# Performance work log

Hardware: AMD Instinct MI355X
Metric: run time of the kernel (lower is better)

Reference implementation:

```python
import jax, jax.numpy as jnp
import numpy as np

B, N, M = 8, 4096, 4096

def _sqdist(x, y):
    # x: [B,N,3], y: [B,M,3] -> squared euclidean distances [B,N,M]
    return jnp.sum((x[:, :, None, :] - y[:, None, :, :]) ** 2, axis=-1)

def _approx_match(xyz1, xyz2):
    # Faithful port of Fan et al. approxmatch.cu (used by PyTorchEMD's
    # earth_mover_distance): annealed soft-assignment over 10 levels.
    b, n, _ = xyz1.shape
    m = xyz2.shape[1]
    d2 = _sqdist(xyz1, xyz2)                      # [B,N,M]
    factorl = max(n, m) / n
    factorr = max(n, m) / m
    satl = jnp.full((b, n), factorl, d2.dtype)    # remaining mass, left
    satr = jnp.full((b, m), factorr, d2.dtype)    # remaining mass, right
    match = jnp.zeros_like(d2)
    # levels: -4^7 .. -4^-1, then 0 (exactly as in approxmatch.cu)
    levels = [-(4.0 ** j) for j in range(7, -2, -1)] + [0.0]
    for level in levels:
        w = jnp.exp(level * d2) * satr[:, None, :]                 # [B,N,M]
        w = w * (satl / (jnp.sum(w, axis=2) + 1e-9))[:, :, None]   # row normalize
        ss2 = jnp.sum(w, axis=1)                                   # [B,M]
        ratio = jnp.minimum(satr / (ss2 + 1e-9), 1.0)
        w = w * ratio[:, None, :]                                  # col capacity clamp
        match = match + w
        satl = jnp.maximum(satl - jnp.sum(w, axis=2), 0.0)
        satr = jnp.maximum(satr - ss2 * ratio, 0.0)
    return match, d2

def setup_inputs() -> dict:
    key = jax.random.key(0)
    k1, k2 = jax.random.split(key)
    array1 = jax.random.uniform(k1, (B, N, 3), dtype=jnp.float32)
    array2 = jax.random.uniform(k2, (B, M, 3), dtype=jnp.float32)
    return {"array1": array1, "array2": array2}

def reference(array1, array2):
    match, d2 = _approx_match(array1, array2)
    dist = jnp.sum(match * d2, axis=(1, 2))   # per-batch EMD (squared-dist transport cost), [B]
    return jnp.mean(dist) / array1.shape[1]
```

## Files before the change

kernel.cpp:

```cpp
#include <hip/hip_runtime.h>


#define BB 8
#define NN 4096
#define MM 4096
#define NPTS 4096

constexpr int   BLK   = 256;
constexpr int   S     = 16;
constexpr int   R     = 4;
constexpr int   RPB   = (BLK / S) * R;
constexpr int   CHUNK = 2048;
constexpr int   G     = (CHUNK / S) / 4;
constexpr float TAU   = 1e-8f;

#if defined(__has_builtin)
#if __has_builtin(__builtin_amdgcn_exp2f)
#define EXP2F(x) __builtin_amdgcn_exp2f(x)
#endif
#if __has_builtin(__builtin_amdgcn_logf)
#define LOG2F(x) __builtin_amdgcn_logf(x)
#endif
#endif
#ifndef EXP2F
#define EXP2F(x) exp2f(x)
#endif
#ifndef LOG2F
#define LOG2F(x) log2f(x)
#endif

__global__ void emd_sort(const float* __restrict__ x1, const float* __restrict__ x2,
                         float* __restrict__ s1, float* __restrict__ s2) {
    __shared__ int hist[64];
    __shared__ int cur[64];
    const int blk = blockIdx.x;
    const float* src = (blk < BB) ? x1 + (size_t)blk * NPTS * 3
                                  : x2 + (size_t)(blk - BB) * NPTS * 3;
    float* dst = (blk < BB) ? s1 + (size_t)blk * NPTS * 3
                            : s2 + (size_t)(blk - BB) * NPTS * 3;
    for (int i = threadIdx.x; i < 64; i += BLK) hist[i] = 0;
    __syncthreads();
    for (int i = threadIdx.x; i < NPTS; i += BLK) {
        float x = src[3*i], y = src[3*i+1], z = src[3*i+2];
        int cx = (int)(x * 4.0f); cx = cx < 0 ? 0 : (cx > 3 ? 3 : cx);
        int cy = (int)(y * 4.0f); cy = cy < 0 ? 0 : (cy > 3 ? 3 : cy);
        int cz = (int)(z * 4.0f); cz = cz < 0 ? 0 : (cz > 3 ? 3 : cz);
        atomicAdd(&hist[(cx << 4) | (cy << 2) | cz], 1);
    }
    __syncthreads();
    if (threadIdx.x == 0) {
        int acc = 0;
        for (int k = 0; k < 64; ++k) { cur[k] = acc; acc += hist[k]; }
    }
    __syncthreads();
    for (int i = threadIdx.x; i < NPTS; i += BLK) {
        float x = src[3*i], y = src[3*i+1], z = src[3*i+2];
        int cx = (int)(x * 4.0f); cx = cx < 0 ? 0 : (cx > 3 ? 3 : cx);
        int cy = (int)(y * 4.0f); cy = cy < 0 ? 0 : (cy > 3 ? 3 : cy);
        int cz = (int)(z * 4.0f); cz = cz < 0 ? 0 : (cz > 3 ? 3 : cz);
        int idx = atomicAdd(&cur[(cx << 4) | (cy << 2) | cz], 1);
        dst[3*idx] = x; dst[3*idx+1] = y; dst[3*idx+2] = z;
    }
}

__global__ void emd_bbox_all(const float* __restrict__ x1s,
                             const float* __restrict__ x2s,
                             float* __restrict__ bb1_16, float* __restrict__ bb1_64,
                             float* __restrict__ bb2_16, float* __restrict__ bb2_64) {
    const int PER = BB * 256 + BB * 64;
    int id = blockIdx.x;
    int cloud = id / PER, r = id % PER;
    const float* xs = cloud ? x2s : x1s;
    float* bb; int gp, grp;
    if (r < BB * 256) { gp = 16; grp = r; bb = cloud ? bb2_16 : bb1_16; }
    else             { gp = 64; grp = r - BB * 256; bb = cloud ? bb2_64 : bb1_64; }
    const int lane = threadIdx.x;
    float xlo = 1e30f, xhi = -1e30f, ylo = 1e30f, yhi = -1e30f,
          zlo = 1e30f, zhi = -1e30f;
    if (lane < gp) {
        const float* p = xs + ((size_t)grp * gp + lane) * 3;
        xlo = xhi = p[0]; ylo = yhi = p[1]; zlo = zhi = p[2];
    }
    #pragma unroll
    for (int d = 1; d < 64; d <<= 1) {
        xlo = fminf(xlo, __shfl_xor(xlo, d)); xhi = fmaxf(xhi, __shfl_xor(xhi, d));
        ylo = fminf(ylo, __shfl_xor(ylo, d)); yhi = fmaxf(yhi, __shfl_xor(yhi, d));
        zlo = fminf(zlo, __shfl_xor(zlo, d)); zhi = fmaxf(zhi, __shfl_xor(zhi, d));
    }
    if (lane == 0) {
        float* o = bb + (size_t)grp * 6;
        o[0]=xlo; o[1]=xhi; o[2]=ylo; o[3]=yhi; o[4]=zlo; o[5]=zhi;
    }
}

__global__ void emd_init(float* __restrict__ satl, float* __restrict__ satr,
                         float* __restrict__ bsum, float* __restrict__ slsum,
                         float* __restrict__ scal, float* __restrict__ out) {
    int i = blockIdx.x * blockDim.x + threadIdx.x;
    if (i < BB * NN) satl[i] = 1.0f;
    if (i < BB * MM) satr[i] = 1.0f;
    if (i < BB)      bsum[i] = 0.0f;
    if (i < BB)      slsum[i] = 0.0f;
    if (i < BB * 5)  scal[i] = 0.0f;
    if (i == 0)      out[0]  = 0.0f;
}

__global__ void compact_all(const float* __restrict__ xyz1s,
                            const float* __restrict__ xyz2s,
                            const float* __restrict__ satl,
                            const float* __restrict__ satr,
                            float* __restrict__ sl,
                            float4* __restrict__ rowBuf, int* __restrict__ rIdx,
                            int* __restrict__ rCnt,
                            float4* __restrict__ colBuf, int* __restrict__ cIdx,
                            int* __restrict__ cCnt) {
    __shared__ int cnts[BLK];
    const bool isRow = blockIdx.x >= BB;
    const int b = isRow ? (blockIdx.x - BB) : blockIdx.x;
    const int PER = NPTS / BLK;
    const float* sb = (isRow ? satl : satr) + (size_t)b * NPTS;
    const float* xb = (isRow ? xyz1s : xyz2s) + (size_t)b * NPTS * 3;
    float* slb = sl + (size_t)b * NN;
    const int st = threadIdx.x * PER;
    int c = 0;
    for (int i = 0; i < PER; ++i) c += (sb[st + i] > TAU) ? 1 : 0;
    cnts[threadIdx.x] = c;
    __syncthreads();
    for (int d = 1; d < BLK; d <<= 1) {
        int v = cnts[threadIdx.x];
        int u = (threadIdx.x >= d) ? cnts[threadIdx.x - d] : 0;
        __syncthreads();
        cnts[threadIdx.x] = v + u;
        __syncthreads();
    }
    const int total = cnts[BLK - 1];
    int off = cnts[threadIdx.x] - c;
    if (isRow) {
        for (int i = 0; i < PER; ++i) {
            int n = st + i;
            if (sb[n] > TAU) {
                rowBuf[(size_t)b * NN + off] =
                    make_float4(xb[3*n], xb[3*n+1], xb[3*n+2], slb[n]);
                rIdx[(size_t)b * NN + off] = n;
                ++off;
            } else if (slb[n] != 0.0f) {
                slb[n] = 0.0f;
            }
        }
        for (int i = total + threadIdx.x; i < NN; i += BLK) {
            rowBuf[(size_t)b * NN + i] = make_float4(0.f, 0.f, 0.f, 0.f);
            rIdx[(size_t)b * NN + i] = 0;
        }
        if (threadIdx.x == 0) rCnt[b] = total;
    } else {
        for (int i = 0; i < PER; ++i) {
            int m = st + i;
            if (sb[m] > TAU) {
                colBuf[(size_t)b * MM + off] =
                    make_float4(xb[3*m], xb[3*m+1], xb[3*m+2], sb[m]);
                cIdx[(size_t)b * MM + off] = m;
                ++off;
            }
        }
        for (int i = total + threadIdx.x; i < MM; i += BLK) {
            colBuf[(size_t)b * MM + i] = make_float4(0.f, 0.f, 0.f, 0.f);
            cIdx[(size_t)b * MM + i] = 0;
        }
        if (threadIdx.x == 0) cCnt[b] = total;
    }
}

#define AB_LOAD(vv, gg)                                          \
    _Pragma("unroll")                                            \
    for (int k = 0; k < 4; ++k) vv[k] = q[((gg)*4 + k)*S + s];

#define AB_COMP(vv)                                              \
    _Pragma("unroll")                                            \
    for (int k = 0; k < 4; ++k) {                                \
        float4 v = vv[k];                                        \
        _Pragma("unroll")                                        \
        for (int r = 0; r < R; ++r) {                            \
            float a0 = v.w + cpp[r];                             \
            float a1 = fmaf(zs[r], v.z, a0);                     \
            float a2 = fmaf(ys[r], v.y, a1);                     \
            float arg = fmaf(xs[r], v.x, a2);                    \
            acc[r] += EXP2F(arg);                                \
        }                                                        \
    }

#define RED_S(v)                                                 \
    v += __shfl_xor(v, 1);  v += __shfl_xor(v, 2);               \
    v += __shfl_xor(v, 4);  v += __shfl_xor(v, 8);

#define RED_W(v)                                                 \
    v += __shfl_xor(v, 1);  v += __shfl_xor(v, 2);               \
    v += __shfl_xor(v, 4);  v += __shfl_xor(v, 8);               \
    v += __shfl_xor(v, 16); v += __shfl_xor(v, 32);

#define BOX_SETUP(rbb)                                           \
    const float* rb = (rbb) + (size_t)(b * 256 + tile * 4 + (threadIdx.x >> 6)) * 6; \
    const float rx0 = rb[0], rx1 = rb[1], ry0 = rb[2], ry1 = rb[3], \
                rz0 = rb[4], rz1 = rb[5];

#define BOX_D2M(cbb, c0, gs, d2m)                                \
    const float* cb = (cbb) + (size_t)(b * 64 + ((c0) >> 6) + (gs)) * 6; \
    float gx = fmaxf(0.0f, fmaxf(cb[0] - rx1, rx0 - cb[1]));     \
    float gy = fmaxf(0.0f, fmaxf(cb[2] - ry1, ry0 - cb[3]));     \
    float gz = fmaxf(0.0f, fmaxf(cb[4] - rz1, rz0 - cb[5]));     \
    float d2m = fmaf(gx, gx, fmaf(gy, gy, gz * gz));

__global__ __launch_bounds__(BLK, 2) void emd_passA_p(
        const float* __restrict__ xyz1, const float* __restrict__ xyz2,
        const float* __restrict__ satl, const float* __restrict__ satr,
        float* __restrict__ sl, const float* __restrict__ rbb,
        const float* __restrict__ cbb, float c, float T) {
    __shared__ float4 q[CHUNK];
    const int b    = blockIdx.x / (NN / RPB);
    const int tile = blockIdx.x % (NN / RPB);
    const float* x2b = xyz2 + (size_t)b * MM * 3;
    const float* srb = satr + (size_t)b * MM;

    const int g = threadIdx.x / S, s = threadIdx.x % S;
    const int n0 = tile * RPB + g * R;
    const float* p = xyz1 + ((size_t)b * NN + n0) * 3;
    const float m2c = -2.0f * c;
    float xs[R], ys[R], zs[R], cpp[R], acc[R];
    #pragma unroll
    for (int r = 0; r < R; ++r) {
        float x = p[3*r], y = p[3*r+1], z = p[3*r+2];
        cpp[r] = c * (x*x + y*y + z*z);
        xs[r] = m2c * x; ys[r] = m2c * y; zs[r] = m2c * z;
        acc[r] = 0.0f;
    }
    BOX_SETUP(rbb);

    for (int c0 = 0; c0 < MM; c0 += CHUNK) {
        __syncthreads();
        for (int m = threadIdx.x; m < CHUNK; m += BLK) {
            int mm = c0 + m;
            float xx = x2b[3*mm], yy = x2b[3*mm+1], zz = x2b[3*mm+2];
            float qq = xx*xx + yy*yy + zz*zz;
            q[m] = make_float4(xx, yy, zz, fmaf(c, qq, LOG2F(srb[mm])));
        }
        __syncthreads();
        for (int gs = 0; gs < G; ++gs) {
            BOX_D2M(cbb, c0, gs, d2m);
            if (d2m > T) continue;
            float4 va[4];
            AB_LOAD(va, gs);
            AB_COMP(va);
        }
    }
    #pragma unroll
    for (int r = 0; r < R; ++r) { RED_S(acc[r]); }
    if (s == 0) {
        #pragma unroll
        for (int r = 0; r < R; ++r) {
            int gi = b * NN + n0 + r;
            sl[gi] = satl[gi] / (acc[r] + 1e-9f);
        }
    }
}

__global__ __launch_bounds__(BLK, 2) void emd_passB_p(
        const float* __restrict__ xyz1, const float* __restrict__ xyz2,
        const float* __restrict__ sl, float* __restrict__ satr,
        float* __restrict__ sr2, const float* __restrict__ rbb,
        const float* __restrict__ cbb, float c, float T) {
    __shared__ float4 q[CHUNK];
    const int b    = blockIdx.x / (MM / RPB);
    const int tile = blockIdx.x % (MM / RPB);
    const float* x1b = xyz1 + (size_t)b * NN * 3;
    const float* slb = sl + (size_t)b * NN;

    const int g = threadIdx.x / S, s = threadIdx.x % S;
    const int m0 = tile * RPB + g * R;
    const float* qp = xyz2 + ((size_t)b * MM + m0) * 3;
    const float m2c = -2.0f * c;
    float xs[R], ys[R], zs[R], cpp[R], acc[R];
    #pragma unroll
    for (int r = 0; r < R; ++r) {
        float x = qp[3*r], y = qp[3*r+1], z = qp[3*r+2];
        cpp[r] = c * (x*x + y*y + z*z);
        xs[r] = m2c * x; ys[r] = m2c * y; zs[r] = m2c * z;
        acc[r] = 0.0f;
    }
    BOX_SETUP(rbb);

    for (int c0 = 0; c0 < NN; c0 += CHUNK) {
        __syncthreads();
        for (int n = threadIdx.x; n < CHUNK; n += BLK) {
            int nn = c0 + n;
            float xx = x1b[3*nn], yy = x1b[3*nn+1], zz = x1b[3*nn+2];
            float pp = xx*xx + yy*yy + zz*zz;
            q[n] = make_float4(xx, yy, zz, fmaf(c, pp, LOG2F(slb[nn])));
        }
        __syncthreads();
        for (int gs = 0; gs < G; ++gs) {
            BOX_D2M(cbb, c0, gs, d2m);
            if (d2m > T) continue;
            float4 va[4];
            AB_LOAD(va, gs);
            AB_COMP(va);
        }
    }
    #pragma unroll
    for (int r = 0; r < R; ++r) { RED_S(acc[r]); }
    if (s == 0) {
        #pragma unroll
        for (int r = 0; r < R; ++r) {
            int gi = b * MM + m0 + r;
            float sr    = satr[gi];
            float ss2   = acc[r] * sr;
            float ratio = fminf(sr / (ss2 + 1e-9f), 1.0f);
            float sn    = fmaxf(sr - ss2 * ratio, 0.0f);
            sr2[gi]  = sr * ratio;
            satr[gi] = sn;
        }
    }
}

#define CA0_LOAD(vv, ww, gg)                                     \
    _Pragma("unroll")                                            \
    for (int k = 0; k < 4; ++k) {                                \
        int idx = ((gg)*4 + k)*S + s;                            \
        vv[k] = q[idx]; ww[k] = w[idx];                          \
    }

#define CA0_COMP(vv, ww)                                         \
    _Pragma("unroll")                                            \
    for (int k = 0; k < 4; ++k) {                                \
        float4 v = vv[k]; float2 wv = ww[k];                     \
        _Pragma("unroll")                                        \
        for (int r = 0; r < R; ++r) {                            \
            float a0 = v.w + cnpp[r];                            \
            float a1 = fmaf(zs[r], v.z, a0);                     \
            float a2 = fmaf(ys[r], v.y, a1);                     \
            float arg = fmaf(xs[r], v.x, a2);                    \
            float en  = EXP2F(arg);                              \
            acc2[r] = fmaf(en, wv.y, acc2[r]);                   \
            float e2 = en * en;                                  \
            float t  = (e2 * e2) * wv.x;                         \
            rd[r]   += t;                                        \
            costA[r] = fmaf(t, arg, costA[r]);                   \
        }                                                        \
    }

#define CA0_COMP_AONLY(vv, ww)                                   \
    _Pragma("unroll")                                            \
    for (int k = 0; k < 4; ++k) {                                \
        float4 v = vv[k]; float2 wv = ww[k];                     \
        _Pragma("unroll")                                        \
        for (int r = 0; r < R; ++r) {                            \
            float a0 = v.w + cnpp[r];                            \
            float a1 = fmaf(zs[r], v.z, a0);                     \
            float a2 = fmaf(ys[r], v.y, a1);                     \
            float arg = fmaf(xs[r], v.x, a2);                    \
            float en  = EXP2F(arg);                              \
            acc2[r] = fmaf(en, wv.y, acc2[r]);                   \
        }                                                        \
    }

__global__ __launch_bounds__(BLK, 2) void emd_passCA0_p(
        const float* __restrict__ xyz1, const float* __restrict__ xyz2,
        float* __restrict__ sl, float* __restrict__ satl,
        const float* __restrict__ sr2, const float* __restrict__ satr_next,
        float* __restrict__ out, const float* __restrict__ rbb,
        const float* __restrict__ cbb, float cl, float cn,
        float T, float TC) {
    __shared__ float4 q[CHUNK];
    __shared__ float2 w[CHUNK];
    const int b    = blockIdx.x / (NN / RPB);
    const int tile = blockIdx.x % (NN / RPB);
    const float* x2b = xyz2 + (size_t)b * MM * 3;
    const float* s2b = sr2 + (size_t)b * MM;
    const float* srb = satr_next + (size_t)b * MM;

    const int g = threadIdx.x / S, s = threadIdx.x % S;
    const int n0 = tile * RPB + g * R;
    const float* pp_ = xyz1 + ((size_t)b * NN + n0) * 3;
    const float m2cn = -2.0f * cn;
    const float icn  = 1.0f / cn;
    float xs[R], ys[R], zs[R], cnpp[R], rd[R], costA[R], acc2[R], slv[R];
    #pragma unroll
    for (int r = 0; r < R; ++r) {
        float x = pp_[3*r], y = pp_[3*r+1], z = pp_[3*r+2];
        cnpp[r] = cn * (x*x + y*y + z*z);
        xs[r] = m2cn * x; ys[r] = m2cn * y; zs[r] = m2cn * z;
        rd[r] = 0.0f; costA[r] = 0.0f; acc2[r] = 0.0f;
        slv[r] = sl[b * NN + n0 + r];
    }
    BOX_SETUP(rbb);

    for (int c0 = 0; c0 < MM; c0 += CHUNK) {
        __syncthreads();
        for (int m = threadIdx.x; m < CHUNK; m += BLK) {
            int mm = c0 + m;
            float xx = x2b[3*mm], yy = x2b[3*mm+1], zz = x2b[3*mm+2];
            float qq = xx*xx + yy*yy + zz*zz;
            q[m] = make_float4(xx, yy, zz, cn * qq);
            w[m] = make_float2(s2b[mm], srb[mm]);
        }
        __syncthreads();
        for (int gs = 0; gs < G; ++gs) {
            BOX_D2M(cbb, c0, gs, d2m);
            if (d2m > T) continue;
            float4 va[4]; float2 wa[4];
            CA0_LOAD(va, wa, gs);
            if (d2m > TC) {
                CA0_COMP_AONLY(va, wa);
            } else {
                CA0_COMP(va, wa);
            }
        }
    }

    #pragma unroll
    for (int r = 0; r < R; ++r) { RED_S(rd[r]); RED_S(acc2[r]); }

    float csum = 0.0f;
    #pragma unroll
    for (int r = 0; r < R; ++r) csum += (costA[r] * icn) * slv[r];
    RED_W(csum);
    if ((threadIdx.x & 63) == 0)
        atomicAdd(out, csum * (1.0f / (float)(BB * NN)));

    if (s == 0) {
        #pragma unroll
        for (int r = 0; r < R; ++r) {
            int gi = b * NN + n0 + r;
            float sa = fmaxf(satl[gi] - rd[r] * slv[r], 0.0f);
            satl[gi] = sa;
            sl[gi] = sa / (acc2[r] + 1e-9f);
        }
    }
}

__global__ __launch_bounds__(BLK, 2) void emd_passB_c(
        const float4* __restrict__ colBuf, const int* __restrict__ cIdx,
        const int* __restrict__ cCnt, const float4* __restrict__ rowBuf,
        const int* __restrict__ rCnt, float* __restrict__ satr,
        float* __restrict__ sr2c, float* __restrict__ satrnc,
        float* __restrict__ bsum, int do_sum, float c) {
    __shared__ float4 q[CHUNK];
    const int b    = blockIdx.x / (MM / RPB);
    const int tile = blockIdx.x % (MM / RPB);
    const int Mc = cCnt[b], Nc = rCnt[b];
    if (tile * RPB >= Mc) return;
    const float4* rb = rowBuf + (size_t)b * NN;

    const int g = threadIdx.x / S, s = threadIdx.x % S;
    const int m0 = tile * RPB + g * R;
    const float m2c = -2.0f * c;
    float xs[R], ys[R], zs[R], cpp[R], acc[R], srv[R];
    #pragma unroll
    for (int r = 0; r < R; ++r) {
        float4 cv = colBuf[(size_t)b * MM + m0 + r];
        srv[r] = cv.w;
        cpp[r] = c * (cv.x*cv.x + cv.y*cv.y + cv.z*cv.z);
        xs[r] = m2c * cv.x; ys[r] = m2c * cv.y; zs[r] = m2c * cv.z;
        acc[r] = 0.0f;
    }

    const int nch = (Nc + CHUNK - 1) / CHUNK;
    for (int ci = 0; ci < nch; ++ci) {
        const int c0 = ci * CHUNK;
        __syncthreads();
        for (int n = threadIdx.x; n < CHUNK; n += BLK) {
            int nn = c0 + n;
            if (nn < Nc) {
                float4 rv = rb[nn];
                float pp = rv.x*rv.x + rv.y*rv.y + rv.z*rv.z;
                q[n] = make_float4(rv.x, rv.y, rv.z, fmaf(c, pp, LOG2F(rv.w)));
            } else {
                q[n] = make_float4(0.f, 0.f, 0.f, -1e30f);
            }
        }
        __syncthreads();
        int rem = Nc - c0; if (rem > CHUNK) rem = CHUNK;
        const int Gact = (rem + S*4 - 1) / (S*4);
        float4 va[4], vb[4];
        AB_LOAD(va, 0);
        #pragma unroll 1
        for (int gs = 0; gs < Gact; gs += 2) {
            if (gs + 1 < Gact) { AB_LOAD(vb, gs + 1); }
            AB_COMP(va);
            if (gs + 2 < Gact) { AB_LOAD(va, gs + 2); }
            if (gs + 1 < Gact) { AB_COMP(vb); }
        }
    }
    #pragma unroll
    for (int r = 0; r < R; ++r) { RED_S(acc[r]); }
    float part = 0.0f;
    if (s == 0) {
        #pragma unroll
        for (int r = 0; r < R; ++r) {
            if (m0 + r < Mc) {
                float sr    = srv[r];
                float ss2   = acc[r] * sr;
                float ratio = fminf(sr / (ss2 + 1e-9f), 1.0f);
                float sn    = fmaxf(sr - ss2 * ratio, 0.0f);
                size_t ci2 = (size_t)b * MM + m0 + r;
                sr2c[ci2]   = sr * ratio;
                satrnc[ci2] = sn;
                satr[(size_t)b * MM + cIdx[ci2]] = sn;
                part += sn;
            }
        }
    }
    if (do_sum) {
        RED_W(part);
        if ((threadIdx.x & 63) == 0) atomicAdd(&bsum[b], part);
    }
}

__global__ __launch_bounds__(BLK, 2) void emd_passCA0_c(
        const float4* __restrict__ rowBuf, const int* __restrict__ rIdx,
        const int* __restrict__ rCnt, const float4* __restrict__ colBuf,
        const int* __restrict__ cCnt, const float* __restrict__ sr2c,
        const float* __restrict__ satrnc, float* __restrict__ satl,
        float* __restrict__ sl, float* __restrict__ out, float cl, float cn) {
    __shared__ float4 q[CHUNK];
    __shared__ float2 w[CHUNK];
    const int b    = blockIdx.x / (NN / RPB);
    const int tile = blockIdx.x % (NN / RPB);
    const int Nc = rCnt[b], Mc = cCnt[b];
    if (tile * RPB >= Nc) return;
    const float4* cbp = colBuf + (size_t)b * MM;
    const float* s2p = sr2c + (size_t)b * MM;
    const float* snp = satrnc + (size_t)b * MM;

    const int g = threadIdx.x / S, s = threadIdx.x % S;
    const int n0 = tile * RPB + g * R;
    const float m2cn = -2.0f * cn;
    const float icn  = 1.0f / cn;
    float xs[R], ys[R], zs[R], cnpp[R], rd[R], costA[R], acc2[R], slv[R];
    #pragma unroll
    for (int r = 0; r < R; ++r) {
        float4 rv = rowBuf[(size_t)b * NN + n0 + r];
        slv[r] = rv.w;
        cnpp[r] = cn * (rv.x*rv.x + rv.y*rv.y + rv.z*rv.z);
        xs[r] = m2cn * rv.x; ys[r] = m2cn * rv.y; zs[r] = m2cn * rv.z;
        rd[r] = 0.0f; costA[r] = 0.0f; acc2[r] = 0.0f;
    }

    const int nch = (Mc + CHUNK - 1) / CHUNK;
    for (int ci = 0; ci < nch; ++ci) {
        const int c0 = ci * CHUNK;
        __syncthreads();
        for (int m = threadIdx.x; m < CHUNK; m += BLK) {
            int mm = c0 + m;
            if (mm < Mc) {
                float4 cv = cbp[mm];
                float qq = cv.x*cv.x + cv.y*cv.y + cv.z*cv.z;
                q[m] = make_float4(cv.x, cv.y, cv.z, cn * qq);
                w[m] = make_float2(s2p[mm], snp[mm]);
            } else {
                q[m] = make_float4(0.f, 0.f, 0.f, 0.f);
                w[m] = make_float2(0.f, 0.f);
            }
        }
        __syncthreads();
        int rem = Mc - c0; if (rem > CHUNK) rem = CHUNK;
        const int Gact = (rem + S*4 - 1) / (S*4);
        float4 va[4], vb[4]; float2 wa[4], wb[4];
        CA0_LOAD(va, wa, 0);
        #pragma unroll 1
        for (int gs = 0; gs < Gact; gs += 2) {
            if (gs + 1 < Gact) { CA0_LOAD(vb, wb, gs + 1); }
            CA0_COMP(va, wa);
            if (gs + 2 < Gact) { CA0_LOAD(va, wa, gs + 2); }
            if (gs + 1 < Gact) { CA0_COMP(vb, wb); }
        }
    }

    #pragma unroll
    for (int r = 0; r < R; ++r) { RED_S(rd[r]); RED_S(acc2[r]); }

    float csum = 0.0f;
    #pragma unroll
    for (int r = 0; r < R; ++r) csum += (costA[r] * icn) * slv[r];
    RED_W(csum);
    if ((threadIdx.x & 63) == 0)
        atomicAdd(out, csum * (1.0f / (float)(BB * NN)));

    if (s == 0) {
        #pragma unroll
        for (int r = 0; r < R; ++r) {
            if (n0 + r < Nc) {
                int gi = b * NN + rIdx[(size_t)b * NN + n0 + r];
                float sa = fmaxf(satl[gi] - rd[r] * slv[r], 0.0f);
                satl[gi] = sa;
                sl[gi] = sa / (acc2[r] + 1e-9f);
            }
        }
    }
}

#define CA1_LOAD(vv, aa, gg)                                     \
    _Pragma("unroll")                                            \
    for (int k = 0; k < 4; ++k) {                                \
        int idx = ((gg)*4 + k)*S + s;                            \
        vv[k] = q[idx]; aa[k] = qa[idx];                         \
    }

#define CA1_COMP(vv, aa)                                         \
    _Pragma("unroll")                                            \
    for (int k = 0; k < 4; ++k) {                                \
        float4 v = vv[k]; float lw = aa[k];                      \
        _Pragma("unroll")                                        \
        for (int r = 0; r < R; ++r) {                            \
            float a0 = v.w + clpp[r];                            \
            float a1 = fmaf(zs[r], v.z, a0);                     \
            float a2 = fmaf(ys[r], v.y, a1);                     \
            float arg = fmaf(xs[r], v.x, a2);                    \
            float t   = EXP2F(arg);                              \
            rd[r] += t;                                          \
            c1[r] = fmaf(t, arg, c1[r]);                         \
            c2[r] = fmaf(t, lw, c2[r]);                          \
        }                                                        \
    }

__global__ __launch_bounds__(BLK, 2) void emd_passCA1_c(
        const float4* __restrict__ rowBuf, const int* __restrict__ rIdx,
        const int* __restrict__ rCnt, const float4* __restrict__ colBuf,
        const int* __restrict__ cCnt, const float* __restrict__ sr2c,
        float* __restrict__ satl, float* __restrict__ sl,
        const float* __restrict__ bsum, float* __restrict__ slsum,
        float* __restrict__ out, float cl) {
    __shared__ float4 q[CHUNK];
    __shared__ float  qa[CHUNK];
    const int b    = blockIdx.x / (NN / RPB);
    const int tile = blockIdx.x % (NN / RPB);
    const int Nc = rCnt[b], Mc = cCnt[b];
    if (tile * RPB >= Nc) return;
    const float4* cbp = colBuf + (size_t)b * MM;
    const float* s2p = sr2c + (size_t)b * MM;

    const int g = threadIdx.x / S, s = threadIdx.x % S;
    const int n0 = tile * RPB + g * R;
    const float m2cl = -2.0f * cl;
    const float icl  = 1.0f / cl;
    float xs[R], ys[R], zs[R], clpp[R], rd[R], c1[R], c2[R], slv[R];
    #pragma unroll
    for (int r = 0; r < R; ++r) {
        float4 rv = rowBuf[(size_t)b * NN + n0 + r];
        slv[r] = rv.w;
        clpp[r] = cl * (rv.x*rv.x + rv.y*rv.y + rv.z*rv.z);
        xs[r] = m2cl * rv.x; ys[r] = m2cl * rv.y; zs[r] = m2cl * rv.z;
        rd[r] = 0.0f; c1[r] = 0.0f; c2[r] = 0.0f;
    }

    const int nch = (Mc + CHUNK - 1) / CHUNK;
    for (int ci = 0; ci < nch; ++ci) {
        const int c0 = ci * CHUNK;
        __syncthreads();
        for (int m = threadIdx.x; m < CHUNK; m += BLK) {
            int mm = c0 + m;
            if (mm < Mc) {
                float4 cv = cbp[mm];
                float qq = cv.x*cv.x + cv.y*cv.y + cv.z*cv.z;
                float lw = LOG2F(fmaxf(s2p[mm], 1e-30f));
                q[m]  = make_float4(cv.x, cv.y, cv.z, fmaf(cl, qq, lw));
                qa[m] = lw;
            } else {
                q[m]  = make_float4(0.f, 0.f, 0.f, -1e30f);
                qa[m] = 0.f;
            }
        }
        __syncthreads();
        int rem = Mc - c0; if (rem > CHUNK) rem = CHUNK;
        const int Gact = (rem + S*4 - 1) / (S*4);
        float4 va[4], vb[4]; float aa[4], ab[4];
        CA1_LOAD(va, aa, 0);
        #pragma unroll 1
        for (int gs = 0; gs < Gact; gs += 2) {
            if (gs + 1 < Gact) { CA1_LOAD(vb, ab, gs + 1); }
            CA1_COMP(va, aa);
            if (gs + 2 < Gact) { CA1_LOAD(va, aa, gs + 2); }
            if (gs + 1 < Gact) { CA1_COMP(vb, ab); }
        }
    }

    #pragma unroll
    for (int r = 0; r < R; ++r) { RED_S(rd[r]); }

    float csum = 0.0f;
    #pragma unroll
    for (int r = 0; r < R; ++r) csum += ((c1[r] - c2[r]) * icl) * slv[r];
    RED_W(csum);
    if ((threadIdx.x & 63) == 0)
        atomicAdd(out, csum * (1.0f / (float)(BB * NN)));

    float part = 0.0f;
    if (s == 0) {
        float bs = bsum[b];
        #pragma unroll
        for (int r = 0; r < R; ++r) {
            if (n0 + r < Nc) {
                int gi = b * NN + rIdx[(size_t)b * NN + n0 + r];
                float sa = fmaxf(satl[gi] - rd[r] * slv[r], 0.0f);
                satl[gi] = sa;
                float s9 = sa / (bs + 1e-9f);
                sl[gi] = s9;
                part += s9;
            }
        }
    }
    RED_W(part);
    if ((threadIdx.x & 63) == 0) atomicAdd(&slsum[b], part);
}

__global__ void emd_lvl9_col(const float* __restrict__ xyz2,
                             const float* __restrict__ satr,
                             const float* __restrict__ slsum,
                             float* __restrict__ scal) {
    int i = blockIdx.x * blockDim.x + threadIdx.x;
    int b = i / MM;
    const float* qp = xyz2 + (size_t)i * 3;
    float sr = satr[i];
    float ss2 = sr * slsum[b];
    float ratio = fminf(sr / (ss2 + 1e-9f), 1.0f);
    float s2 = sr * ratio;
    float x = qp[0], y = qp[1], z = qp[2];
    float v0 = s2, v1 = s2*x, v2 = s2*y, v3 = s2*z;
    float v4 = s2 * (x*x + y*y + z*z);
    #pragma unroll
    for (int d = 1; d < 64; d <<= 1) {
        v0 += __shfl_xor(v0, d); v1 += __shfl_xor(v1, d);
        v2 += __shfl_xor(v2, d); v3 += __shfl_xor(v3, d);
        v4 += __shfl_xor(v4, d);
    }
    if ((threadIdx.x & 63) == 0) {
        atomicAdd(&scal[b*5+0], v0); atomicAdd(&scal[b*5+1], v1);
        atomicAdd(&scal[b*5+2], v2); atomicAdd(&scal[b*5+3], v3);
        atomicAdd(&scal[b*5+4], v4);
    }
}

__global__ void emd_lvl9_cost(const float* __restrict__ xyz1,
                              const float* __restrict__ sl,
                              const float* __restrict__ scal,
                              float* __restrict__ out) {
    int i = blockIdx.x * blockDim.x + threadIdx.x;
    int b = i / NN;
    float W  = scal[b*5+0], Wx = scal[b*5+1], Wy = scal[b*5+2];
    float Wz = scal[b*5+3], Q  = scal[b*5+4];
    const float* p = xyz1 + (size_t)i * 3;
    float x = p[0], y = p[1], z = p[2];
    float pp = x*x + y*y + z*z;
    float dotw = x*Wx + y*Wy + z*Wz;
    float c = sl[i] * (pp * W + Q - 2.0f * dotw);
    #pragma unroll
    for (int d = 1; d < 64; d <<= 1) c += __shfl_xor(c, d);
    if ((threadIdx.x & 63) == 0)
        atomicAdd(out, c * (1.0f / (float)(BB * NN)));
}

extern "C" void kernel_launch(void* const* d_in, const int* in_sizes, int n_in,
                              void* d_out, int out_size, void* d_ws, size_t ws_size,
                              hipStream_t stream) {
    const float* xyz1 = (const float*)d_in[0];
    const float* xyz2 = (const float*)d_in[1];
    float* out  = (float*)d_out;

    float* satl   = (float*)d_ws;
    float* sl     = satl  + BB * NN;
    float* satr   = sl    + BB * NN;
    float* sr2    = satr  + BB * MM;
    float* bsum   = sr2   + BB * MM;
    float* slsum  = bsum  + BB;
    float* scal   = slsum + BB;
    float* xyz1s  = scal  + BB * 5;
    float* xyz2s  = xyz1s + BB * NN * 3;
    float* bb1_16 = xyz2s + BB * MM * 3;
    float* bb1_64 = bb1_16 + BB * 256 * 6;
    float* bb2_16 = bb1_64 + BB * 64 * 6;
    float* bb2_64 = bb2_16 + BB * 256 * 6;
    float4* rowBuf = (float4*)(bb2_64 + BB * 64 * 6);
    float4* colBuf = rowBuf + BB * NN;
    float* sr2c   = (float*)(colBuf + BB * MM);
    float* satrnc = sr2c  + BB * MM;
    int*   rIdx   = (int*)(satrnc + BB * MM);
    int*   cIdx   = rIdx  + BB * NN;
    int*   rCnt   = cIdx  + BB * MM;
    int*   cCnt   = rCnt  + BB;

    emd_sort<<<2 * BB, BLK, 0, stream>>>(xyz1, xyz2, xyz1s, xyz2s);
    emd_bbox_all<<<2 * (BB * 256 + BB * 64), 64, 0, stream>>>(
        xyz1s, xyz2s, bb1_16, bb1_64, bb2_16, bb2_64);
    emd_init<<<(BB * NN + 255) / 256, 256, 0, stream>>>(satl, satr, bsum,
                                                        slsum, scal, out);

    const double levels[10] = {-16384.0, -4096.0, -1024.0, -256.0, -64.0,
                               -16.0, -4.0, -1.0, -0.25, 0.0};
    const double LOG2E = 1.4426950408889634;
    float c[10], T[10];
    for (int l = 0; l < 10; ++l) {
        c[l] = (float)(levels[l] * LOG2E);
        T[l] = (l < 9) ? (float)(80.0 / (-levels[l] * LOG2E)) : 1e30f;
    }

    const int grid = BB * (NN / RPB);

    emd_passA_p<<<grid, BLK, 0, stream>>>(xyz1s, xyz2s, satl, satr, sl,
                                          bb1_16, bb2_64, c[0], T[0]);
    for (int l = 0; l <= 2; ++l) {
        emd_passB_p<<<grid, BLK, 0, stream>>>(xyz1s, xyz2s, sl, satr, sr2,
                                              bb2_16, bb1_64, c[l], T[l]);
        emd_passCA0_p<<<grid, BLK, 0, stream>>>(
            xyz1s, xyz2s, sl, satl, sr2, satr, out, bb1_16, bb2_64,
            c[l], c[l + 1], T[l + 1], T[l]);
    }

    compact_all<<<2 * BB, BLK, 0, stream>>>(xyz1s, xyz2s, satl, satr, sl,
                                            rowBuf, rIdx, rCnt,
                                            colBuf, cIdx, cCnt);
    for (int l = 3; l <= 8; ++l) {
        emd_passB_c<<<grid, BLK, 0, stream>>>(colBuf, cIdx, cCnt, rowBuf, rCnt,
                                              satr, sr2c, satrnc, bsum,
                                              (l == 8) ? 1 : 0, c[l]);
        if (l < 8) {
            emd_passCA0_c<<<grid, BLK, 0, stream>>>(
                rowBuf, rIdx, rCnt, colBuf, cCnt, sr2c, satrnc,
                satl, sl, out, c[l], c[l + 1]);
            compact_all<<<2 * BB, BLK, 0, stream>>>(xyz1s, xyz2s, satl, satr, sl,
                                                    rowBuf, rIdx, rCnt,
                                                    colBuf, cIdx, cCnt);
        } else {
            emd_passCA1_c<<<grid, BLK, 0, stream>>>(
                rowBuf, rIdx, rCnt, colBuf, cCnt, sr2c,
                satl, sl, bsum, slsum, out, c[8]);
        }
    }
    emd_lvl9_col<<<BB * MM / 256, 256, 0, stream>>>(xyz2s, satr, slsum, scal);
    emd_lvl9_cost<<<BB * NN / 256, 256, 0, stream>>>(xyz1s, sl, scal, out);
}
```

Measured before the change: 721.9 us.

## Compute bounding boxes on compacted buffers and prune level-3 tiles

The compaction kernel now also builds 16- and 64-point bounding boxes over the compacted row and column buffers, and pads the tail with the last valid coordinate so the boxes stay tight. The schedule changes: level 2 ends with a separate passC on the full arrays, and after the first compaction a separate passA is launched. Level 3 then uses template-enabled box pruning in passB and passCA0, skipping groups whose minimum distance exceeds the exp cutoff. The intent is to drop exp work for far-apart point groups at level 3. In exchange there are extra launches and per-group branch overhead, and the double-buffered loads are lost in the pruned path.

```diff
diff --git a/kernel.cpp b/kernel.cpp
--- a/kernel.cpp
+++ b/kernel.cpp
@@ -113,7 +113,9 @@
                             float4* __restrict__ rowBuf, int* __restrict__ rIdx,
                             int* __restrict__ rCnt,
                             float4* __restrict__ colBuf, int* __restrict__ cIdx,
-                            int* __restrict__ cCnt) {
+                            int* __restrict__ cCnt,
+                            float* __restrict__ rb16c, float* __restrict__ rb64c,
+                            float* __restrict__ cb16c, float* __restrict__ cb64c) {
     __shared__ int cnts[BLK];
     const bool isRow = blockIdx.x >= BB;
     const int b = isRow ? (blockIdx.x - BB) : blockIdx.x;
@@ -121,6 +123,8 @@
     const float* sb = (isRow ? satl : satr) + (size_t)b * NPTS;
     const float* xb = (isRow ? xyz1s : xyz2s) + (size_t)b * NPTS * 3;
     float* slb = sl + (size_t)b * NN;
+    float4* buf = isRow ? (rowBuf + (size_t)b * NN) : (colBuf + (size_t)b * MM);
+    int*    idx = isRow ? (rIdx + (size_t)b * NN)   : (cIdx + (size_t)b * MM);
     const int st = threadIdx.x * PER;
     int c = 0;
     for (int i = 0; i < PER; ++i) c += (sb[st + i] > TAU) ? 1 : 0;
@@ -139,34 +143,58 @@
         for (int i = 0; i < PER; ++i) {
             int n = st + i;
             if (sb[n] > TAU) {
-                rowBuf[(size_t)b * NN + off] =
-                    make_float4(xb[3*n], xb[3*n+1], xb[3*n+2], slb[n]);
-                rIdx[(size_t)b * NN + off] = n;
+                buf[off] = make_float4(xb[3*n], xb[3*n+1], xb[3*n+2], slb[n]);
+                idx[off] = n;
                 ++off;
             } else if (slb[n] != 0.0f) {
                 slb[n] = 0.0f;
             }
         }
-        for (int i = total + threadIdx.x; i < NN; i += BLK) {
-            rowBuf[(size_t)b * NN + i] = make_float4(0.f, 0.f, 0.f, 0.f);
-            rIdx[(size_t)b * NN + i] = 0;
-        }
-        if (threadIdx.x == 0) rCnt[b] = total;
     } else {
         for (int i = 0; i < PER; ++i) {
             int m = st + i;
             if (sb[m] > TAU) {
-                colBuf[(size_t)b * MM + off] =
-                    make_float4(xb[3*m], xb[3*m+1], xb[3*m+2], sb[m]);
-                cIdx[(size_t)b * MM + off] = m;
+                buf[off] = make_float4(xb[3*m], xb[3*m+1], xb[3*m+2], sb[m]);
+                idx[off] = m;
                 ++off;
             }
         }
-        for (int i = total + threadIdx.x; i < MM; i += BLK) {
-            colBuf[(size_t)b * MM + i] = make_float4(0.f, 0.f, 0.f, 0.f);
-            cIdx[(size_t)b * MM + i] = 0;
-        }
-        if (threadIdx.x == 0) cCnt[b] = total;
+    }
+    for (int i = total + threadIdx.x; i < NPTS; i += BLK) idx[i] = 0;
+    __syncthreads();
+    float4 lastv = make_float4(0.f, 0.f, 0.f, 0.f);
+    if (total > 0) lastv = buf[total - 1];
+    for (int i = total + threadIdx.x; i < NPTS; i += BLK)
+        buf[i] = make_float4(lastv.x, lastv.y, lastv.z, 0.0f);
+    if (threadIdx.x == 0) { if (isRow) rCnt[b] = total; else cCnt[b] = total; }
+    __syncthreads();
+    float* b16 = (isRow ? rb16c : cb16c) + (size_t)b * 256 * 6;
+    float* b64 = (isRow ? rb64c : cb64c) + (size_t)b * 64 * 6;
+    {
+        int g16 = threadIdx.x;
+        float xlo = 1e30f, xhi = -1e30f, ylo = 1e30f, yhi = -1e30f,
+              zlo = 1e30f, zhi = -1e30f;
+        for (int i = 0; i < 16; ++i) {
+            float4 v = buf[g16 * 16 + i];
+            xlo = fminf(xlo, v.x); xhi = fmaxf(xhi, v.x);
+            ylo = fminf(ylo, v.y); yhi = fmaxf(yhi, v.y);
+            zlo = fminf(zlo, v.z); zhi = fmaxf(zhi, v.z);
+        }
+        float* o = b16 + (size_t)g16 * 6;
+        o[0]=xlo; o[1]=xhi; o[2]=ylo; o[3]=yhi; o[4]=zlo; o[5]=zhi;
+    }
+    __syncthreads();
+    if (threadIdx.x < 64) {
+        float xlo = 1e30f, xhi = -1e30f, ylo = 1e30f, yhi = -1e30f,
+              zlo = 1e30f, zhi = -1e30f;
+        for (int k = 0; k < 4; ++k) {
+            float* i16 = b16 + (size_t)(threadIdx.x * 4 + k) * 6;
+            xlo = fminf(xlo, i16[0]); xhi = fmaxf(xhi, i16[1]);
+            ylo = fminf(ylo, i16[2]); yhi = fmaxf(yhi, i16[3]);
+            zlo = fminf(zlo, i16[4]); zhi = fmaxf(zhi, i16[5]);
+        }
+        float* o = b64 + (size_t)threadIdx.x * 6;
+        o[0]=xlo; o[1]=xhi; o[2]=ylo; o[3]=yhi; o[4]=zlo; o[5]=zhi;
     }
 }
 
@@ -436,18 +464,170 @@
     }
 }
 
+#define C_COMP1(v, lw)                                           \
+    { _Pragma("unroll")                                          \
+      for (int r = 0; r < R; ++r) {                              \
+        float a0 = (v).w + clpp[r];                              \
+        float a1 = fmaf(zs[r], (v).z, a0);                       \
+        float a2 = fmaf(ys[r], (v).y, a1);                       \
+        float arg = fmaf(xs[r], (v).x, a2);                      \
+        float t   = EXP2F(arg);                                  \
+        rd[r] += t;                                              \
+        c1[r] = fmaf(t, arg, c1[r]);                             \
+        c2[r] = fmaf(t, (lw), c2[r]);                            \
+      } }
+
+__global__ __launch_bounds__(BLK, 2) void emd_passC_p(
+        const float* __restrict__ xyz1, const float* __restrict__ xyz2,
+        const float* __restrict__ sl, float* __restrict__ satl,
+        const float* __restrict__ sr2, float* __restrict__ out,
+        const float* __restrict__ rbb, const float* __restrict__ cbb,
+        float cl, float T) {
+    __shared__ float4 q[CHUNK];
+    __shared__ float  qa[CHUNK];
+    const int b    = blockIdx.x / (NN / RPB);
+    const int tile = blockIdx.x % (NN / RPB);
+    const float* x2b = xyz2 + (size_t)b * MM * 3;
+    const float* s2b = sr2 + (size_t)b * MM;
+
+    const int g = threadIdx.x / S, s = threadIdx.x % S;
+    const int n0 = tile * RPB + g * R;
+    const float* pp_ = xyz1 + ((size_t)b * NN + n0) * 3;
+    const float m2cl = -2.0f * cl;
+    const float icl  = 1.0f / cl;
+    float xs[R], ys[R], zs[R], clpp[R], rd[R], c1[R], c2[R], slv[R];
+    #pragma unroll
+    for (int r = 0; r < R; ++r) {
+        float x = pp_[3*r], y = pp_[3*r+1], z = pp_[3*r+2];
+        clpp[r] = cl * (x*x + y*y + z*z);
+        xs[r] = m2cl * x; ys[r] = m2cl * y; zs[r] = m2cl * z;
+        rd[r] = 0.0f; c1[r] = 0.0f; c2[r] = 0.0f;
+        slv[r] = sl[b * NN + n0 + r];
+    }
+    BOX_SETUP(rbb);
+
+    for (int c0 = 0; c0 < MM; c0 += CHUNK) {
+        __syncthreads();
+        for (int m = threadIdx.x; m < CHUNK; m += BLK) {
+            int mm = c0 + m;
+            float xx = x2b[3*mm], yy = x2b[3*mm+1], zz = x2b[3*mm+2];
+            float qq = xx*xx + yy*yy + zz*zz;
+            float lw = LOG2F(fmaxf(s2b[mm], 1e-30f));
+            q[m]  = make_float4(xx, yy, zz, fmaf(cl, qq, lw));
+            qa[m] = lw;
+        }
+        __syncthreads();
+        for (int gs = 0; gs < G; ++gs) {
+            BOX_D2M(cbb, c0, gs, d2m);
+            if (d2m > T) continue;
+            #pragma unroll
+            for (int k = 0; k < 4; ++k) {
+                int idx = (gs*4 + k)*S + s;
+                float4 v = q[idx]; float lw = qa[idx];
+                C_COMP1(v, lw);
+            }
+        }
+    }
+
+    #pragma unroll
+    for (int r = 0; r < R; ++r) { RED_S(rd[r]); }
+
+    float csum = 0.0f;
+    #pragma unroll
+    for (int r = 0; r < R; ++r) csum += ((c1[r] - c2[r]) * icl) * slv[r];
+    RED_W(csum);
+    if ((threadIdx.x & 63) == 0)
+        atomicAdd(out, csum * (1.0f / (float)(BB * NN)));
+
+    if (s == 0) {
+        #pragma unroll
+        for (int r = 0; r < R; ++r) {
+            int gi = b * NN + n0 + r;
+            satl[gi] = fmaxf(satl[gi] - rd[r] * slv[r], 0.0f);
+        }
+    }
+}
+
+__global__ __launch_bounds__(BLK, 2) void emd_passA_c(
+        float4* __restrict__ rowBuf, const int* __restrict__ rIdx,
+        const int* __restrict__ rCnt, const float4* __restrict__ colBuf,
+        const int* __restrict__ cCnt, const float* __restrict__ satl,
+        float* __restrict__ sl, const float* __restrict__ rbbC,
+        const float* __restrict__ cbbC, float c, float T) {
+    __shared__ float4 q[CHUNK];
+    const int b    = blockIdx.x / (NN / RPB);
+    const int tile = blockIdx.x % (NN / RPB);
+    const int Nc = rCnt[b], Mc = cCnt[b];
+    if (tile * RPB >= Nc) return;
+    const float4* cbp = colBuf + (size_t)b * MM;
+
+    const int g = threadIdx.x / S, s = threadIdx.x % S;
+    const int n0 = tile * RPB + g * R;
+    const float m2c = -2.0f * c;
+    float xs[R], ys[R], zs[R], cpp[R], acc[R];
+    #pragma unroll
+    for (int r = 0; r < R; ++r) {
+        float4 rv = rowBuf[(size_t)b * NN + n0 + r];
+        cpp[r] = c * (rv.x*rv.x + rv.y*rv.y + rv.z*rv.z);
+        xs[r] = m2c * rv.x; ys[r] = m2c * rv.y; zs[r] = m2c * rv.z;
+        acc[r] = 0.0f;
+    }
+    BOX_SETUP(rbbC);
+
+    const int nch = (Mc + CHUNK - 1) / CHUNK;
+    for (int ci = 0; ci < nch; ++ci) {
+        const int c0 = ci * CHUNK;
+        __syncthreads();
+        for (int m = threadIdx.x; m < CHUNK; m += BLK) {
+            int mm = c0 + m;
+            if (mm < Mc) {
+                float4 cv = cbp[mm];
+                float qq = cv.x*cv.x + cv.y*cv.y + cv.z*cv.z;
+                q[m] = make_float4(cv.x, cv.y, cv.z, fmaf(c, qq, LOG2F(cv.w)));
+            } else {
+                q[m] = make_float4(0.f, 0.f, 0.f, -1e30f);
+            }
+        }
+        __syncthreads();
+        int rem = Mc - c0; if (rem > CHUNK) rem = CHUNK;
+        const int Gact = (rem + S*4 - 1) / (S*4);
+        for (int gs = 0; gs < Gact; ++gs) {
+            BOX_D2M(cbbC, c0, gs, d2m);
+            if (d2m > T) continue;
+            float4 va[4];
+            AB_LOAD(va, gs);
+            AB_COMP(va);
+        }
+    }
+    #pragma unroll
+    for (int r = 0; r < R; ++r) { RED_S(acc[r]); }
+    if (s == 0) {
+        #pragma unroll
+        for (int r = 0; r < R; ++r) {
+            if (n0 + r < Nc) {
+                int gi = b * NN + rIdx[(size_t)b * NN + n0 + r];
+                float v = satl[gi] / (acc[r] + 1e-9f);
+                sl[gi] = v;
+                ((float*)&rowBuf[(size_t)b * NN + n0 + r])[3] = v;
+            }
+        }
+    }
+}
+
+template<int PRUNE>
 __global__ __launch_bounds__(BLK, 2) void emd_passB_c(
         const float4* __restrict__ colBuf, const int* __restrict__ cIdx,
         const int* __restrict__ cCnt, const float4* __restrict__ rowBuf,
         const int* __restrict__ rCnt, float* __restrict__ satr,
         float* __restrict__ sr2c, float* __restrict__ satrnc,
-        float* __restrict__ bsum, int do_sum, float c) {
+        float* __restrict__ bsum, const float* __restrict__ rbbC,
+        const float* __restrict__ cbbC, int do_sum, float c, float T) {
     __shared__ float4 q[CHUNK];
     const int b    = blockIdx.x / (MM / RPB);
     const int tile = blockIdx.x % (MM / RPB);
     const int Mc = cCnt[b], Nc = rCnt[b];
     if (tile * RPB >= Mc) return;
-    const float4* rb = rowBuf + (size_t)b * NN;
+    const float4* rb_ = rowBuf + (size_t)b * NN;
 
     const int g = threadIdx.x / S, s = threadIdx.x % S;
     const int m0 = tile * RPB + g * R;
@@ -461,6 +641,7 @@
         xs[r] = m2c * cv.x; ys[r] = m2c * cv.y; zs[r] = m2c * cv.z;
         acc[r] = 0.0f;
     }
+    BOX_SETUP(rbbC);
 
     const int nch = (Nc + CHUNK - 1) / CHUNK;
     for (int ci = 0; ci < nch; ++ci) {
@@ -469,7 +650,7 @@
         for (int n = threadIdx.x; n < CHUNK; n += BLK) {
             int nn = c0 + n;
             if (nn < Nc) {
-                float4 rv = rb[nn];
+                float4 rv = rb_[nn];
                 float pp = rv.x*rv.x + rv.y*rv.y + rv.z*rv.z;
                 q[n] = make_float4(rv.x, rv.y, rv.z, fmaf(c, pp, LOG2F(rv.w)));
             } else {
@@ -479,14 +660,24 @@
         __syncthreads();
         int rem = Nc - c0; if (rem > CHUNK) rem = CHUNK;
         const int Gact = (rem + S*4 - 1) / (S*4);
-        float4 va[4], vb[4];
-        AB_LOAD(va, 0);
-        #pragma unroll 1
-        for (int gs = 0; gs < Gact; gs += 2) {
-            if (gs + 1 < Gact) { AB_LOAD(vb, gs + 1); }
-            AB_COMP(va);
-            if (gs + 2 < Gact) { AB_LOAD(va, gs + 2); }
-            if (gs + 1 < Gact) { AB_COMP(vb); }
+        if (PRUNE) {
+            for (int gs = 0; gs < Gact; ++gs) {
+                BOX_D2M(cbbC, c0, gs, d2m);
+                if (d2m > T) continue;
+                float4 va[4];
+                AB_LOAD(va, gs);
+                AB_COMP(va);
+            }
+        } else {
+            float4 va[4], vb[4];
+            AB_LOAD(va, 0);
+            #pragma unroll 1
+            for (int gs = 0; gs < Gact; gs += 2) {
+                if (gs + 1 < Gact) { AB_LOAD(vb, gs + 1); }
+                AB_COMP(va);
+                if (gs + 2 < Gact) { AB_LOAD(va, gs + 2); }
+                if (gs + 1 < Gact) { AB_COMP(vb); }
+            }
         }
     }
     #pragma unroll
@@ -514,12 +705,15 @@
     }
 }
 
+template<int PRUNE>
 __global__ __launch_bounds__(BLK, 2) void emd_passCA0_c(
         const float4* __restrict__ rowBuf, const int* __restrict__ rIdx,
         const int* __restrict__ rCnt, const float4* __restrict__ colBuf,
         const int* __restrict__ cCnt, const float* __restrict__ sr2c,
         const float* __restrict__ satrnc, float* __restrict__ satl,
-        float* __restrict__ sl, float* __restrict__ out, float cl, float cn) {
+        float* __restrict__ sl, float* __restrict__ out,
+        const float* __restrict__ rbbC, const float* __restrict__ cbbC,
+        float cl, float cn, float T, float TC) {
     __shared__ float4 q[CHUNK];
     __shared__ float2 w[CHUNK];
     const int b    = blockIdx.x / (NN / RPB);
@@ -543,6 +737,7 @@
         xs[r] = m2cn * rv.x; ys[r] = m2cn * rv.y; zs[r] = m2cn * rv.z;
         rd[r] = 0.0f; costA[r] = 0.0f; acc2[r] = 0.0f;
     }
+    BOX_SETUP(rbbC);
 
     const int nch = (Mc + CHUNK - 1) / CHUNK;
     for (int ci = 0; ci < nch; ++ci) {
@@ -563,14 +758,28 @@
         __syncthreads();
         int rem = Mc - c0; if (rem > CHUNK) rem = CHUNK;
         const int Gact = (rem + S*4 - 1) / (S*4);
-        float4 va[4], vb[4]; float2 wa[4], wb[4];
-        CA0_LOAD(va, wa, 0);
-        #pragma unroll 1
-        for (int gs = 0; gs < Gact; gs += 2) {
-            if (gs + 1 < Gact) { CA0_LOAD(vb, wb, gs + 1); }
-            CA0_COMP(va, wa);
-            if (gs + 2 < Gact) { CA0_LOAD(va, wa, gs + 2); }
-            if (gs + 1 < Gact) { CA0_COMP(vb, wb); }
+        if (PRUNE) {
+            for (int gs = 0; gs < Gact; ++gs) {
+                BOX_D2M(cbbC, c0, gs, d2m);
+                if (d2m > T) continue;
+                float4 va[4]; float2 wa[4];
+                CA0_LOAD(va, wa, gs);
+                if (d2m > TC) {
+                    CA0_COMP_AONLY(va, wa);
+                } else {
+                    CA0_COMP(va, wa);
+                }
+            }
+        } else {
+            float4 va[4], vb[4]; float2 wa[4], wb[4];
+            CA0_LOAD(va, wa, 0);
+            #pragma unroll 1
+            for (int gs = 0; gs < Gact; gs += 2) {
+                if (gs + 1 < Gact) { CA0_LOAD(vb, wb, gs + 1); }
+                CA0_COMP(va, wa);
+                if (gs + 2 < Gact) { CA0_LOAD(va, wa, gs + 2); }
+                if (gs + 1 < Gact) { CA0_COMP(vb, wb); }
+            }
         }
     }
 
@@ -579,7 +788,8 @@
 
     float csum = 0.0f;
     #pragma unroll
-    for (int r = 0; r < R; ++r) csum += (costA[r] * icn) * slv[r];
+    for (int r = 0; r < R; ++r)
+        csum += (n0 + r < Nc) ? (costA[r] * icn) * slv[r] : 0.0f;
     RED_W(csum);
     if ((threadIdx.x & 63) == 0)
         atomicAdd(out, csum * (1.0f / (float)(BB * NN)));
@@ -687,7 +897,8 @@
 
     float csum = 0.0f;
     #pragma unroll
-    for (int r = 0; r < R; ++r) csum += ((c1[r] - c2[r]) * icl) * slv[r];
+    for (int r = 0; r < R; ++r)
+        csum += (n0 + r < Nc) ? ((c1[r] - c2[r]) * icl) * slv[r] : 0.0f;
     RED_W(csum);
     if ((threadIdx.x & 63) == 0)
         atomicAdd(out, csum * (1.0f / (float)(BB * NN)));
@@ -785,6 +996,10 @@
     int*   cIdx   = rIdx  + BB * NN;
     int*   rCnt   = cIdx  + BB * MM;
     int*   cCnt   = rCnt  + BB;
+    float* rb16c  = (float*)(cCnt + BB);
+    float* rb64c  = rb16c + BB * 256 * 6;
+    float* cb16c  = rb64c + BB * 64 * 6;
+    float* cb64c  = cb16c + BB * 256 * 6;
 
     emd_sort<<<2 * BB, BLK, 0, stream>>>(xyz1, xyz2, xyz1s, xyz2s);
     emd_bbox_all<<<2 * (BB * 256 + BB * 64), 64, 0, stream>>>(
@@ -805,28 +1020,49 @@
 
     emd_passA_p<<<grid, BLK, 0, stream>>>(xyz1s, xyz2s, satl, satr, sl,
                                           bb1_16, bb2_64, c[0], T[0]);
-    for (int l = 0; l <= 2; ++l) {
+    for (int l = 0; l <= 1; ++l) {
         emd_passB_p<<<grid, BLK, 0, stream>>>(xyz1s, xyz2s, sl, satr, sr2,
                                               bb2_16, bb1_64, c[l], T[l]);
         emd_passCA0_p<<<grid, BLK, 0, stream>>>(
             xyz1s, xyz2s, sl, satl, sr2, satr, out, bb1_16, bb2_64,
             c[l], c[l + 1], T[l + 1], T[l]);
     }
+    emd_passB_p<<<grid, BLK, 0, stream>>>(xyz1s, xyz2s, sl, satr, sr2,
+                                          bb2_16, bb1_64, c[2], T[2]);
+    emd_passC_p<<<grid, BLK, 0, stream>>>(xyz1s, xyz2s, sl, satl, sr2, out,
+                                          bb1_16, bb2_64, c[2], T[2]);
 
     compact_all<<<2 * BB, BLK, 0, stream>>>(xyz1s, xyz2s, satl, satr, sl,
                                             rowBuf, rIdx, rCnt,
-                                            colBuf, cIdx, cCnt);
+                                            colBuf, cIdx, cCnt,
+                                            rb16c, rb64c, cb16c, cb64c);
+    emd_passA_c<<<grid, BLK, 0, stream>>>(rowBuf, rIdx, rCnt, colBuf, cCnt,
+                                          satl, sl, rb16c, cb64c, c[3], T[3]);
+
     for (int l = 3; l <= 8; ++l) {
-        emd_passB_c<<<grid, BLK, 0, stream>>>(colBuf, cIdx, cCnt, rowBuf, rCnt,
-                                              satr, sr2c, satrnc, bsum,
-                                              (l == 8) ? 1 : 0, c[l]);
+        if (l == 3)
+            emd_passB_c<1><<<grid, BLK, 0, stream>>>(
+                colBuf, cIdx, cCnt, rowBuf, rCnt, satr, sr2c, satrnc, bsum,
+                cb16c, rb64c, 0, c[l], T[l]);
+        else
+            emd_passB_c<0><<<grid, BLK, 0, stream>>>(
+                colBuf, cIdx, cCnt, rowBuf, rCnt, satr, sr2c, satrnc, bsum,
+                cb16c, rb64c, (l == 8) ? 1 : 0, c[l], 1e30f);
         if (l < 8) {
-            emd_passCA0_c<<<grid, BLK, 0, stream>>>(
-                rowBuf, rIdx, rCnt, colBuf, cCnt, sr2c, satrnc,
-                satl, sl, out, c[l], c[l + 1]);
+            if (l == 3)
+                emd_passCA0_c<1><<<grid, BLK, 0, stream>>>(
+                    rowBuf, rIdx, rCnt, colBuf, cCnt, sr2c, satrnc,
+                    satl, sl, out, rb16c, cb64c, c[l], c[l + 1],
+                    T[l + 1], T[l]);
+            else
+                emd_passCA0_c<0><<<grid, BLK, 0, stream>>>(
+                    rowBuf, rIdx, rCnt, colBuf, cCnt, sr2c, satrnc,
+                    satl, sl, out, rb16c, cb64c, c[l], c[l + 1],
+                    1e30f, 1e30f);
             compact_all<<<2 * BB, BLK, 0, stream>>>(xyz1s, xyz2s, satl, satr, sl,
                                                     rowBuf, rIdx, rCnt,
-                                                    colBuf, cIdx, cCnt);
+                                                    colBuf, cIdx, cCnt,
+                                                    rb16c, rb64c, cb16c, cb64c);
         } else {
             emd_passCA1_c<<<grid, BLK, 0, stream>>>(
                 rowBuf, rIdx, rCnt, colBuf, cCnt, sr2c,
```

Result: slower. 766.0 us (+6.1%).
